# Kernel optimization log

Hardware: AMD Instinct MI355X
Metric: run time of the kernel (lower is better)

## Reference

```python
import jax, jax.numpy as jnp
import numpy as np

N = 16_777_216  # number of draft tokens / cache slots
ACCEPT_PROB = 0.7


def setup_inputs() -> dict:
    key = jax.random.key(0)
    k1, k2, k3 = jax.random.split(key, 3)
    idx = jax.random.randint(k1, (N,), 0, N, dtype=jnp.int64)
    keep = jax.random.uniform(k2, (N,)) < ACCEPT_PROB
    # rejected slots are marked -1, as in the original kernel
    accept_index = jnp.where(keep, idx, jnp.int64(-1))
    out_cache_loc = jax.random.normal(k3, (N,), dtype=jnp.float32)
    return {"accept_index": accept_index, "out_cache_loc": out_cache_loc}


def reference(accept_index, out_cache_loc):
    """Stream compaction: gather out_cache_loc[accept_index[i]] for every i with
    accept_index[i] >= 0, packed densely at the front of the output.

    The original returns an array of length num_accepted (data-dependent). For a
    static, jit-compatible shape we return a length-N array whose first
    num_accepted entries equal the original output and the rest are zero.
    """
    n = accept_index.shape[0]
    mask = accept_index >= 0                      # [N] bool
    # exclusive prefix sum of mask = destination slot for each accepted element
    dst = jnp.cumsum(mask.astype(jnp.int64)) - mask.astype(jnp.int64)  # [N]
    # gather (use 0 as a safe dummy index for rejected lanes)
    vals = out_cache_loc[jnp.where(mask, accept_index, 0)]             # [N]
    # scatter accepted values to their compacted slots; rejected lanes are
    # routed to index n, which mode='drop' discards
    scatter_idx = jnp.where(mask, dst, n)
    out = jnp.zeros((n,), dtype=out_cache_loc.dtype)
    out = out.at[scatter_idx].set(vals, mode="drop")
    return out
```

## Files before the change

### kernel.cpp

```cpp
#include <hip/hip_runtime.h>


#define N_TOTAL  16777216
#define BLOCK    256

#define EPT      16
#define TILE     (BLOCK * EPT)
#define NBLOCKS  (N_TOTAL / TILE)

#define EPT2     32
#define TILE2    (BLOCK * EPT2)
#define NB2      (N_TOTAL / TILE2)

#define SLICE_LG 22
#define SLICES   (N_TOTAL >> SLICE_LG)

typedef float vfloat4 __attribute__((ext_vector_type(4)));

__global__ __launch_bounds__(BLOCK) void k_reduce(const int* __restrict__ idx,
                                                  int* __restrict__ blockSums) {
    const int b = blockIdx.x;
    const int t = threadIdx.x;
    const int4* p = (const int4*)(idx + (size_t)b * TILE + (size_t)t * EPT);
    int cnt = 0;
#pragma unroll
    for (int j = 0; j < EPT / 4; ++j) {
        int4 v = p[j];
        cnt += (v.x >= 0) + (v.y >= 0) + (v.z >= 0) + (v.w >= 0);
    }
#pragma unroll
    for (int d = 32; d > 0; d >>= 1) cnt += __shfl_down(cnt, d);
    __shared__ int wsum[BLOCK / 64];
    const int lane = t & 63, wave = t >> 6;
    if (lane == 0) wsum[wave] = cnt;
    __syncthreads();
    if (t == 0) {
        int s = 0;
#pragma unroll
        for (int w = 0; w < BLOCK / 64; ++w) s += wsum[w];
        blockSums[b] = s;
    }
}

__global__ __launch_bounds__(256) void k_scan(const int* __restrict__ blockSums,
                                              int* __restrict__ blockOffsets) {
    const int t = threadIdx.x;
    const int lane = t & 63, wave = t >> 6;
    int vals[16];
    const int4* p = (const int4*)(blockSums + t * 16);
#pragma unroll
    for (int j = 0; j < 4; ++j) {
        int4 v = p[j];
        vals[4 * j + 0] = v.x; vals[4 * j + 1] = v.y;
        vals[4 * j + 2] = v.z; vals[4 * j + 3] = v.w;
    }
    int tsum = 0;
#pragma unroll
    for (int j = 0; j < 16; ++j) tsum += vals[j];

    int x = tsum;
#pragma unroll
    for (int d = 1; d < 64; d <<= 1) {
        int y = __shfl_up(x, d);
        if (lane >= d) x += y;
    }
    __shared__ int wsum[4], woff[4];
    if (lane == 63) wsum[wave] = x;
    __syncthreads();
    if (t == 0) {
        int s = 0;
#pragma unroll
        for (int w = 0; w < 4; ++w) { woff[w] = s; s += wsum[w]; }
        blockOffsets[NBLOCKS] = s;
    }
    __syncthreads();
    int run = (x - tsum) + woff[wave];
#pragma unroll
    for (int j = 0; j < 16; ++j) {
        blockOffsets[t * 16 + j] = run;
        run += vals[j];
    }
}

__global__ __launch_bounds__(BLOCK) void k_scatter(const int* __restrict__ idx,
                                                   const float* __restrict__ src,
                                                   const int* __restrict__ blockOffsets,
                                                   float* __restrict__ out) {
    const int b = blockIdx.x;
    const int t = threadIdx.x;
    const int lane = t & 63, wave = t >> 6;
    const int4* p = (const int4*)(idx + (size_t)b * TILE2 + (size_t)t * EPT2);
    int v[EPT2];
#pragma unroll
    for (int j = 0; j < EPT2 / 4; ++j) {
        int4 q = p[j];
        v[4 * j + 0] = q.x; v[4 * j + 1] = q.y;
        v[4 * j + 2] = q.z; v[4 * j + 3] = q.w;
    }

    int cnt = 0;
#pragma unroll
    for (int j = 0; j < EPT2; ++j) cnt += (v[j] >= 0);

    int x = cnt;
#pragma unroll
    for (int d = 1; d < 64; d <<= 1) {
        int y = __shfl_up(x, d);
        if (lane >= d) x += y;
    }
    __shared__ int wsum[BLOCK / 64], woff[BLOCK / 64];
    __shared__ int btotal;
    if (lane == 63) wsum[wave] = x;
    __syncthreads();
    if (t == 0) {
        int s = 0;
#pragma unroll
        for (int w = 0; w < BLOCK / 64; ++w) { woff[w] = s; s += wsum[w]; }
        btotal = s;
    }
    __syncthreads();
    const int off0 = (x - cnt) + woff[wave];

    __shared__ float vals[TILE2];
#pragma unroll 1
    for (int s = 0; s < SLICES; ++s) {
        float tmp[EPT2];
#pragma unroll
        for (int j = 0; j < EPT2; ++j) {
            const bool m = (int)((unsigned)v[j] >> SLICE_LG) == s;
            tmp[j] = src[m ? v[j] : 0];
        }
        asm volatile("s_waitcnt vmcnt(0)" ::: "memory");
        int o = off0;
#pragma unroll
        for (int j = 0; j < EPT2; ++j) {
            const bool acc = v[j] >= 0;
            const bool m = (int)((unsigned)v[j] >> SLICE_LG) == s;
            if (m) vals[o] = tmp[j];
            o += acc;
        }
    }
    __syncthreads();

    const int base = blockOffsets[2 * b];
    const int tot  = btotal;
    for (int i = t; i < tot; i += BLOCK)
        __builtin_nontemporal_store(vals[i], out + base + i);
}

__global__ __launch_bounds__(256) void k_tail(float* __restrict__ out,
                                              const int* __restrict__ total_p) {
    const int total = *total_p;
    const int i = (blockIdx.x * 256 + threadIdx.x) * 4;
    if (i >= total) {
        vfloat4 z = (vfloat4)(0.f);
        __builtin_nontemporal_store(z, (vfloat4*)(out + i));
    } else if (i + 4 > total) {
#pragma unroll
        for (int k = 0; k < 4; ++k)
            if (i + k >= total) out[i + k] = 0.f;
    }
}

extern "C" void kernel_launch(void* const* d_in, const int* in_sizes, int n_in,
                              void* d_out, int out_size, void* d_ws, size_t ws_size,
                              hipStream_t stream) {
    const int*   idx = (const int*)d_in[0];
    const float* src = (const float*)d_in[1];
    float*       out = (float*)d_out;

    int* blockSums    = (int*)d_ws;
    int* blockOffsets = blockSums + NBLOCKS;

    k_reduce <<<NBLOCKS, BLOCK, 0, stream>>>(idx, blockSums);
    k_scan   <<<1, 256, 0, stream>>>(blockSums, blockOffsets);
    k_scatter<<<NB2, BLOCK, 0, stream>>>(idx, src, blockOffsets, out);
    k_tail   <<<N_TOTAL / 4 / 256, 256, 0, stream>>>(out, blockOffsets + NBLOCKS);
}
```

Measured before the change: 344.1 us.

## Replace reduce-scan-scatter pipeline with single-pass decoupled look-back compaction

Merges the separate count, block-scan, scatter and zero-tail kernels into one compaction kernel. Each block publishes its local aggregate and then an inclusive prefix, looked up by a wave-wide decoupled look-back over a per-block state array. Each block also zero-fills its own share of the rejected tail slots. This removes the extra full read of the index array and the separate tail pass, at the cost of a dependency on blocks being scheduled in order and serial look-back latency, which can spin.

```diff
diff --git a/kernel.cpp b/kernel.cpp
--- a/kernel.cpp
+++ b/kernel.cpp
@@ -3,10 +3,6 @@
 
 #define N_TOTAL  16777216
 #define BLOCK    256
-
-#define EPT      16
-#define TILE     (BLOCK * EPT)
-#define NBLOCKS  (N_TOTAL / TILE)
 
 #define EPT2     32
 #define TILE2    (BLOCK * EPT2)
@@ -17,78 +13,18 @@
 
 typedef float vfloat4 __attribute__((ext_vector_type(4)));
 
-__global__ __launch_bounds__(BLOCK) void k_reduce(const int* __restrict__ idx,
-                                                  int* __restrict__ blockSums) {
-    const int b = blockIdx.x;
-    const int t = threadIdx.x;
-    const int4* p = (const int4*)(idx + (size_t)b * TILE + (size_t)t * EPT);
-    int cnt = 0;
-#pragma unroll
-    for (int j = 0; j < EPT / 4; ++j) {
-        int4 v = p[j];
-        cnt += (v.x >= 0) + (v.y >= 0) + (v.z >= 0) + (v.w >= 0);
-    }
-#pragma unroll
-    for (int d = 32; d > 0; d >>= 1) cnt += __shfl_down(cnt, d);
-    __shared__ int wsum[BLOCK / 64];
-    const int lane = t & 63, wave = t >> 6;
-    if (lane == 0) wsum[wave] = cnt;
-    __syncthreads();
-    if (t == 0) {
-        int s = 0;
-#pragma unroll
-        for (int w = 0; w < BLOCK / 64; ++w) s += wsum[w];
-        blockSums[b] = s;
-    }
+__global__ __launch_bounds__(256) void k_init(unsigned long long* __restrict__ state) {
+    state[blockIdx.x * 256 + threadIdx.x] = 0ULL;
 }
 
-__global__ __launch_bounds__(256) void k_scan(const int* __restrict__ blockSums,
-                                              int* __restrict__ blockOffsets) {
-    const int t = threadIdx.x;
-    const int lane = t & 63, wave = t >> 6;
-    int vals[16];
-    const int4* p = (const int4*)(blockSums + t * 16);
-#pragma unroll
-    for (int j = 0; j < 4; ++j) {
-        int4 v = p[j];
-        vals[4 * j + 0] = v.x; vals[4 * j + 1] = v.y;
-        vals[4 * j + 2] = v.z; vals[4 * j + 3] = v.w;
-    }
-    int tsum = 0;
-#pragma unroll
-    for (int j = 0; j < 16; ++j) tsum += vals[j];
-
-    int x = tsum;
-#pragma unroll
-    for (int d = 1; d < 64; d <<= 1) {
-        int y = __shfl_up(x, d);
-        if (lane >= d) x += y;
-    }
-    __shared__ int wsum[4], woff[4];
-    if (lane == 63) wsum[wave] = x;
-    __syncthreads();
-    if (t == 0) {
-        int s = 0;
-#pragma unroll
-        for (int w = 0; w < 4; ++w) { woff[w] = s; s += wsum[w]; }
-        blockOffsets[NBLOCKS] = s;
-    }
-    __syncthreads();
-    int run = (x - tsum) + woff[wave];
-#pragma unroll
-    for (int j = 0; j < 16; ++j) {
-        blockOffsets[t * 16 + j] = run;
-        run += vals[j];
-    }
-}
-
-__global__ __launch_bounds__(BLOCK) void k_scatter(const int* __restrict__ idx,
+__global__ __launch_bounds__(BLOCK) void k_compact(const int* __restrict__ idx,
                                                    const float* __restrict__ src,
-                                                   const int* __restrict__ blockOffsets,
-                                                   float* __restrict__ out) {
+                                                   float* __restrict__ out,
+                                                   unsigned long long* __restrict__ state) {
     const int b = blockIdx.x;
     const int t = threadIdx.x;
     const int lane = t & 63, wave = t >> 6;
+
     const int4* p = (const int4*)(idx + (size_t)b * TILE2 + (size_t)t * EPT2);
     int v[EPT2];
 #pragma unroll
@@ -97,7 +33,6 @@
         v[4 * j + 0] = q.x; v[4 * j + 1] = q.y;
         v[4 * j + 2] = q.z; v[4 * j + 3] = q.w;
     }
-
     int cnt = 0;
 #pragma unroll
     for (int j = 0; j < EPT2; ++j) cnt += (v[j] >= 0);
@@ -108,8 +43,8 @@
         int y = __shfl_up(x, d);
         if (lane >= d) x += y;
     }
-    __shared__ int wsum[BLOCK / 64], woff[BLOCK / 64];
-    __shared__ int btotal;
+    __shared__ int wsum[BLOCK / 64], woff[BLOCK / 64], btotal;
+    __shared__ long long sBase;
     if (lane == 63) wsum[wave] = x;
     __syncthreads();
     if (t == 0) {
@@ -117,9 +52,55 @@
 #pragma unroll
         for (int w = 0; w < BLOCK / 64; ++w) { woff[w] = s; s += wsum[w]; }
         btotal = s;
+        if (b == 0) {
+            __hip_atomic_store(&state[0], ((unsigned long long)s << 2) | 2ULL,
+                               __ATOMIC_RELAXED, __HIP_MEMORY_SCOPE_AGENT);
+            sBase = 0;
+        } else {
+            __hip_atomic_store(&state[b], ((unsigned long long)s << 2) | 1ULL,
+                               __ATOMIC_RELAXED, __HIP_MEMORY_SCOPE_AGENT);
+        }
+    }
+
+    if (b > 0 && wave == 0) {
+        long long excl = 0;
+        int look = b - 1;
+        for (;;) {
+            const int pos = look - lane;
+            unsigned long long s = 2ULL;
+            if (pos >= 0)
+                s = __hip_atomic_load(&state[pos], __ATOMIC_RELAXED,
+                                      __HIP_MEMORY_SCOPE_AGENT);
+            for (;;) {
+                const bool need = (pos >= 0) && ((s & 3ULL) == 0ULL);
+                if (!__any(need)) break;
+                if (need) {
+                    __builtin_amdgcn_s_sleep(2);
+                    s = __hip_atomic_load(&state[pos], __ATOMIC_RELAXED,
+                                          __HIP_MEMORY_SCOPE_AGENT);
+                }
+            }
+            const unsigned long long ball = __ballot((s & 3ULL) == 2ULL);
+            const int fp = ball ? (__ffsll((long long)ball) - 1) : 64;
+            long long c = (lane <= fp) ? (long long)(s >> 2) : 0;
+#pragma unroll
+            for (int d = 32; d; d >>= 1) c += __shfl_down(c, d);
+            excl += __shfl(c, 0);
+            if (ball) break;
+            look -= 64;
+        }
+        if (lane == 0) {
+            __hip_atomic_store(&state[b],
+                               (((unsigned long long)(excl + btotal)) << 2) | 2ULL,
+                               __ATOMIC_RELAXED, __HIP_MEMORY_SCOPE_AGENT);
+            sBase = excl;
+        }
     }
     __syncthreads();
+
     const int off0 = (x - cnt) + woff[wave];
+    const int tot  = btotal;
+    const long long base = sBase;
 
     __shared__ float vals[TILE2];
 #pragma unroll 1
@@ -142,24 +123,14 @@
     }
     __syncthreads();
 
-    const int base = blockOffsets[2 * b];
-    const int tot  = btotal;
     for (int i = t; i < tot; i += BLOCK)
         __builtin_nontemporal_store(vals[i], out + base + i);
-}
 
-__global__ __launch_bounds__(256) void k_tail(float* __restrict__ out,
-                                              const int* __restrict__ total_p) {
-    const int total = *total_p;
-    const int i = (blockIdx.x * 256 + threadIdx.x) * 4;
-    if (i >= total) {
-        vfloat4 z = (vfloat4)(0.f);
-        __builtin_nontemporal_store(z, (vfloat4*)(out + i));
-    } else if (i + 4 > total) {
-#pragma unroll
-        for (int k = 0; k < 4; ++k)
-            if (i + k >= total) out[i + k] = 0.f;
-    }
+    const long long rprev = (long long)b * TILE2 - base;
+    const int rcnt = TILE2 - tot;
+    float* zp = out + ((long long)N_TOTAL - rprev - rcnt);
+    for (int i = t; i < rcnt; i += BLOCK)
+        __builtin_nontemporal_store(0.0f, zp + i);
 }
 
 extern "C" void kernel_launch(void* const* d_in, const int* in_sizes, int n_in,
@@ -169,11 +140,8 @@
     const float* src = (const float*)d_in[1];
     float*       out = (float*)d_out;
 
-    int* blockSums    = (int*)d_ws;
-    int* blockOffsets = blockSums + NBLOCKS;
+    unsigned long long* state = (unsigned long long*)d_ws;
 
-    k_reduce <<<NBLOCKS, BLOCK, 0, stream>>>(idx, blockSums);
-    k_scan   <<<1, 256, 0, stream>>>(blockSums, blockOffsets);
-    k_scatter<<<NB2, BLOCK, 0, stream>>>(idx, src, blockOffsets, out);
-    k_tail   <<<N_TOTAL / 4 / 256, 256, 0, stream>>>(out, blockOffsets + NBLOCKS);
+    k_init   <<<NB2 / 256, 256, 0, stream>>>(state);
+    k_compact<<<NB2, BLOCK, 0, stream>>>(idx, src, out, state);
 }
```

Result: faster. 321.2 us (-6.7%).
